# Kernel tuning notes

Measured on AMD Instinct MI355X. Metric: run time of the kernel, lower is better.

## Reference

```python
import jax, jax.numpy as jnp
import numpy as np
import math

B, S, D, H = 2, 2048, 1024, 16
DH = D // H


def setup_inputs() -> dict:
    key = jax.random.key(0)
    ks = jax.random.split(key, 10)
    scale = 1.0 / math.sqrt(D)
    inp = {
        "x": jax.random.normal(ks[0], (B, S, D), dtype=jnp.float32),
        "valid_nums": jax.random.randint(ks[1], (B,), 1, S + 1, dtype=jnp.int32),
        "Wq": jax.random.normal(ks[2], (D, D), dtype=jnp.float32) * scale,
        "bq": jnp.zeros((D,), dtype=jnp.float32),
        "Wk": jax.random.normal(ks[3], (D, D), dtype=jnp.float32) * scale,
        "bk": jnp.zeros((D,), dtype=jnp.float32),
        "Wv": jax.random.normal(ks[4], (D, D), dtype=jnp.float32) * scale,
        "bv": jnp.zeros((D,), dtype=jnp.float32),
        "Wo": jax.random.normal(ks[5], (D, D), dtype=jnp.float32) * scale,
        "bo": jnp.zeros((D,), dtype=jnp.float32),
    }
    return inp


def _split_heads(t):
    # (B, S, D) -> (B, H, S, DH)
    return t.reshape(B, S, H, DH).transpose(0, 2, 1, 3)


def reference(x, valid_nums, Wq, bq, Wk, bk, Wv, bv, Wo, bo):
    q = _split_heads(x @ Wq + bq)
    k = _split_heads(x @ Wk + bk)
    v = _split_heads(x @ Wv + bv)
    scores = jnp.einsum("bhqd,bhkd->bhqk", q, k) / math.sqrt(DH)  # (B,H,S,S)
    # length mask over keys: key j valid iff j < valid_nums[b]
    key_mask = jnp.arange(S)[None, :] < valid_nums[:, None]        # (B,S)
    scores = jnp.where(key_mask[:, None, None, :], scores, -jnp.inf)
    attn = jax.nn.softmax(scores, axis=-1)
    out = jnp.einsum("bhqk,bhkd->bhqd", attn, v)                   # (B,H,S,DH)
    out = out.transpose(0, 2, 1, 3).reshape(B, S, D)
    return out @ Wo + bo
```

## Files before the change

### kernel.cpp

```cpp
#include <hip/hip_runtime.h>
#include <hip/hip_bf16.h>
#include <math.h>

static constexpr int Bb = 2, Ss = 2048, Dd = 1024, Hh = 16, DHh = 64;
static constexpr int Mm = Bb * Ss;
static constexpr int Kk = Dd;

typedef __attribute__((ext_vector_type(8))) short bf16x8;
typedef __attribute__((ext_vector_type(4))) float f32x4;
typedef unsigned short us;

__device__ inline short f2b(float f) {
    __hip_bfloat16 h = __float2bfloat16(f);
    return *reinterpret_cast<short*>(&h);
}
__device__ inline float b2f(us u) {
    __hip_bfloat16 h = *reinterpret_cast<__hip_bfloat16*>(&u);
    return __bfloat162float(h);
}
__device__ inline unsigned pk2(float lo, float hi) {
    return ((unsigned)(us)f2b(hi) << 16) | (unsigned)(us)f2b(lo);
}
__device__ inline float ex2(float x) {
    return __builtin_amdgcn_exp2f(x);
}

__device__ inline void gload16(us* lds, const us* g) {
    __builtin_amdgcn_global_load_lds(
        (const __attribute__((address_space(1))) void*)g,
        (__attribute__((address_space(3))) void*)lds,
        16, 0, 0);
}

__global__ __launch_bounds__(256)
void xconv_kernel(const float* __restrict__ x, us* __restrict__ xb)
{
    const size_t i = ((size_t)blockIdx.x * 256 + threadIdx.x) * 8;
    float4 a = *(const float4*)(x + i);
    float4 b = *(const float4*)(x + i + 4);
    bf16x8 t;
    t[0] = f2b(a.x); t[1] = f2b(a.y); t[2] = f2b(a.z); t[3] = f2b(a.w);
    t[4] = f2b(b.x); t[5] = f2b(b.y); t[6] = f2b(b.z); t[7] = f2b(b.w);
    *(bf16x8*)(xb + i) = t;
}

__global__ __launch_bounds__(256)
void wtrans_kernel(const float* __restrict__ Wq, const float* __restrict__ Wk,
                   const float* __restrict__ Wv, const float* __restrict__ Wo,
                   us* __restrict__ Wt, us* __restrict__ Woth, us* __restrict__ Wotl)
{
    __shared__ float T[64][65];
    const int z = blockIdx.z;
    const float* W = (z == 0) ? Wq : (z == 1) ? Wk : (z == 2) ? Wv : Wo;
    const int split = (z == 3);
    us* dh = split ? Woth : (Wt + (size_t)z * Dd * Kk);
    us* dl = Wotl;

    const int n0 = blockIdx.x * 64, k0 = blockIdx.y * 64;
    const int tid = threadIdx.x;
    const int r = tid >> 2, c0 = (tid & 3) * 16;
#pragma unroll
    for (int j = 0; j < 4; ++j) {
        float4 v = *(const float4*)(W + (size_t)(k0 + r) * Dd + n0 + c0 + 4 * j);
        T[r][c0 + 4 * j + 0] = v.x;
        T[r][c0 + 4 * j + 1] = v.y;
        T[r][c0 + 4 * j + 2] = v.z;
        T[r][c0 + 4 * j + 3] = v.w;
    }
    __syncthreads();
    us hi[16], lo[16];
#pragma unroll
    for (int j = 0; j < 16; ++j) {
        float v = T[c0 + j][r];
        us h = (us)f2b(v);
        hi[j] = h;
        if (split) lo[j] = (us)f2b(v - b2f(h));
    }
    *(bf16x8*)&dh[(size_t)(n0 + r) * Kk + k0 + c0]     = *(bf16x8*)&hi[0];
    *(bf16x8*)&dh[(size_t)(n0 + r) * Kk + k0 + c0 + 8] = *(bf16x8*)&hi[8];
    if (split) {
        *(bf16x8*)&dl[(size_t)(n0 + r) * Kk + k0 + c0]     = *(bf16x8*)&lo[0];
        *(bf16x8*)&dl[(size_t)(n0 + r) * Kk + k0 + c0 + 8] = *(bf16x8*)&lo[8];
    }
}

__global__ __launch_bounds__(256)
void gemm_qkv_kernel(const us* __restrict__ xb, const us* __restrict__ Wt,
                     const float* __restrict__ bq, const float* __restrict__ bk,
                     const float* __restrict__ bv, us* __restrict__ QKV)
{
    __shared__ us As[2][128 * 64];
    __shared__ us Bs[2][128 * 64];
    const int tid = threadIdx.x;
    const int wave = tid >> 6, lane = tid & 63;
    const int wr = wave >> 1, wc = wave & 1;
    const int lg = lane >> 4, ll = lane & 15;
    const int col0 = blockIdx.x * 128;
    const int row0 = blockIdx.y * 128;

    f32x4 acc[4][4];
#pragma unroll
    for (int mt = 0; mt < 4; ++mt)
#pragma unroll
        for (int nt = 0; nt < 4; ++nt)
#pragma unroll
            for (int r = 0; r < 4; ++r) acc[mt][nt][r] = 0.f;

    const us* Ag = xb + (size_t)(row0 + wave * 32 + (lane >> 3)) * Kk + (lane & 7) * 8;
    const us* Bg = Wt + (size_t)(col0 + wave * 32 + (lane >> 3)) * Kk + (lane & 7) * 8;
    const int ldsb = (wave * 4) * 512;

#pragma unroll
    for (int i = 0; i < 4; ++i) {
        gload16(&As[0][ldsb + i * 512], Ag + (size_t)(i * 8) * Kk);
        gload16(&Bs[0][ldsb + i * 512], Bg + (size_t)(i * 8) * Kk);
    }
    __syncthreads();

    for (int it = 0; it < 16; ++it) {
        const int sb = it & 1;
        if (it < 15) {
            const int kn = (it + 1) * 64;
#pragma unroll
            for (int i = 0; i < 4; ++i) {
                gload16(&As[sb ^ 1][ldsb + i * 512], Ag + (size_t)(i * 8) * Kk + kn);
                gload16(&Bs[sb ^ 1][ldsb + i * 512], Bg + (size_t)(i * 8) * Kk + kn);
            }
        }
#pragma unroll
        for (int ks = 0; ks < 2; ++ks) {
            bf16x8 af[4], bfr[4];
#pragma unroll
            for (int mt = 0; mt < 4; ++mt)
                af[mt] = *(const bf16x8*)&As[sb][(wr * 64 + mt * 16 + ll) * 64 + ks * 32 + lg * 8];
#pragma unroll
            for (int nt = 0; nt < 4; ++nt)
                bfr[nt] = *(const bf16x8*)&Bs[sb][(wc * 64 + nt * 16 + ll) * 64 + ks * 32 + lg * 8];
#pragma unroll
            for (int mt = 0; mt < 4; ++mt)
#pragma unroll
                for (int nt = 0; nt < 4; ++nt)
                    acc[mt][nt] = __builtin_amdgcn_mfma_f32_16x16x32_bf16(af[mt], bfr[nt], acc[mt][nt], 0, 0, 0);
        }
        __syncthreads();
    }

    const int z = col0 >> 10;
    const int c0 = col0 & 1023;
    const float* bias = (z == 0) ? bq : (z == 1) ? bk : bv;
    const float osc = (z == 0) ? 0.125f * 1.44269504f : 1.0f;
    us* outz = QKV + (size_t)z * Mm * Dd;

    if (z == 2) {
#pragma unroll
        for (int mt = 0; mt < 4; ++mt)
#pragma unroll
            for (int nt = 0; nt < 4; ++nt) {
                int row = row0 + wr * 64 + mt * 16 + lg * 4;
                int col = c0 + wc * 64 + nt * 16 + ll;
                int b_ = row >> 11, s_ = row & 2047;
                float bv_ = bias[col];
                union { us u[4]; uint2 d2; } pk;
#pragma unroll
                for (int r = 0; r < 4; ++r) pk.u[r] = (us)f2b(acc[mt][nt][r] + bv_);
                *(uint2*)&outz[((size_t)(b_ * Hh * DHh) + col) * Ss + s_] = pk.d2;
            }
    } else {
#pragma unroll
        for (int mt = 0; mt < 4; ++mt)
#pragma unroll
            for (int nt = 0; nt < 4; ++nt)
#pragma unroll
                for (int r = 0; r < 4; ++r) {
                    int row = row0 + wr * 64 + mt * 16 + lg * 4 + r;
                    int col = c0 + wc * 64 + nt * 16 + ll;
                    float v = (acc[mt][nt][r] + bias[col]) * osc;
                    int b_ = row >> 11, s_ = row & 2047, h_ = col >> 6, d_ = col & 63;
                    outz[(((size_t)(b_ * Hh + h_)) * Ss + s_) * DHh + d_] = (us)f2b(v);
                }
    }
}

__global__ __launch_bounds__(256)
void gemm_final_kernel(const us* __restrict__ Oh, const us* __restrict__ Ol,
                       const us* __restrict__ Wth, const us* __restrict__ Wtl,
                       const float* __restrict__ bo, float* __restrict__ out)
{
    __shared__ us AhS[128 * 64];
    __shared__ us AlS[128 * 64];
    __shared__ us BhS[64 * 64];
    __shared__ us BlS[64 * 64];
    const int tid = threadIdx.x;
    const int wave = tid >> 6, lane = tid & 63;
    const int wr = wave >> 1, wc = wave & 1;
    const int lg = lane >> 4, ll = lane & 15;
    const int col0 = blockIdx.x * 64;
    const int row0 = blockIdx.y * 128;

    f32x4 acc[4][2];
#pragma unroll
    for (int mt = 0; mt < 4; ++mt)
#pragma unroll
        for (int nt = 0; nt < 2; ++nt)
#pragma unroll
            for (int r = 0; r < 4; ++r) acc[mt][nt][r] = 0.f;

    const size_t aoff = (size_t)(row0 + wave * 32 + (lane >> 3)) * Kk + (lane & 7) * 8;
    const size_t boff = (size_t)(col0 + wave * 16 + (lane >> 3)) * Kk + (lane & 7) * 8;
    const us* Ahg = Oh + aoff;
    const us* Alg = Ol + aoff;
    const us* Bhg = Wth + boff;
    const us* Blg = Wtl + boff;
    us* AhD = &AhS[(wave * 4) * 512];
    us* AlD = &AlS[(wave * 4) * 512];
    us* BhD = &BhS[(wave * 2) * 512];
    us* BlD = &BlS[(wave * 2) * 512];

    for (int k0 = 0; k0 < Kk; k0 += 64) {
        __syncthreads();
#pragma unroll
        for (int i = 0; i < 4; ++i) {
            gload16(AhD + i * 512, Ahg + (size_t)(i * 8) * Kk + k0);
            gload16(AlD + i * 512, Alg + (size_t)(i * 8) * Kk + k0);
        }
#pragma unroll
        for (int j = 0; j < 2; ++j) {
            gload16(BhD + j * 512, Bhg + (size_t)(j * 8) * Kk + k0);
            gload16(BlD + j * 512, Blg + (size_t)(j * 8) * Kk + k0);
        }
        __syncthreads();
#pragma unroll
        for (int ks = 0; ks < 2; ++ks) {
            bf16x8 ah[4], al[4], bh[2], bl[2];
#pragma unroll
            for (int mt = 0; mt < 4; ++mt) {
                ah[mt] = *(const bf16x8*)&AhS[(wr * 64 + mt * 16 + ll) * 64 + ks * 32 + lg * 8];
                al[mt] = *(const bf16x8*)&AlS[(wr * 64 + mt * 16 + ll) * 64 + ks * 32 + lg * 8];
            }
#pragma unroll
            for (int nt = 0; nt < 2; ++nt) {
                bh[nt] = *(const bf16x8*)&BhS[(wc * 32 + nt * 16 + ll) * 64 + ks * 32 + lg * 8];
                bl[nt] = *(const bf16x8*)&BlS[(wc * 32 + nt * 16 + ll) * 64 + ks * 32 + lg * 8];
            }
#pragma unroll
            for (int mt = 0; mt < 4; ++mt)
#pragma unroll
                for (int nt = 0; nt < 2; ++nt) {
                    acc[mt][nt] = __builtin_amdgcn_mfma_f32_16x16x32_bf16(ah[mt], bh[nt], acc[mt][nt], 0, 0, 0);
                    acc[mt][nt] = __builtin_amdgcn_mfma_f32_16x16x32_bf16(al[mt], bh[nt], acc[mt][nt], 0, 0, 0);
                    acc[mt][nt] = __builtin_amdgcn_mfma_f32_16x16x32_bf16(ah[mt], bl[nt], acc[mt][nt], 0, 0, 0);
                }
        }
    }

#pragma unroll
    for (int mt = 0; mt < 4; ++mt)
#pragma unroll
        for (int nt = 0; nt < 2; ++nt)
#pragma unroll
            for (int r = 0; r < 4; ++r) {
                int row = row0 + wr * 64 + mt * 16 + lg * 4 + r;
                int col = col0 + wc * 32 + nt * 16 + ll;
                out[(size_t)row * Dd + col] = acc[mt][nt][r] + bo[col];
            }
}

__global__ __launch_bounds__(512)
void attn_mfma_kernel(const us* __restrict__ Q, const us* __restrict__ K,
                      const us* __restrict__ Vt_g, const int* __restrict__ valid_nums,
                      us* __restrict__ Oh, us* __restrict__ Ol)
{
    const int id  = blockIdx.x;
    const int xcd = id & 7, grp = id >> 3;
    const int bh  = (grp >> 4) * 8 + xcd;
    const int qb  = grp & 15;
    const int b   = bh >> 4, h = bh & 15;
    const int q0  = qb * 128;

    const int tid  = threadIdx.x;
    const int wave = tid >> 6;
    const int lane = tid & 63;
    const int lg = lane >> 4;
    const int ll = lane & 15;

    const int nv = valid_nums[b];
    const int ntiles = (nv + 127) >> 7;

    const us* Qb = Q    + (size_t)bh * Ss * DHh;
    const us* Kb = K    + (size_t)bh * Ss * DHh;
    const us* Vb = Vt_g + (size_t)bh * DHh * Ss;

    __shared__ us Ks[128][72];
    __shared__ us Vs[64][136];

    bf16x8 qa[2];
    {
        const us* qrow = Qb + (size_t)(q0 + wave * 16 + ll) * DHh;
        qa[0] = *(const bf16x8*)(qrow + lg * 8);
        qa[1] = *(const bf16x8*)(qrow + 32 + lg * 8);
    }

    union { unsigned w[4]; bf16x8 v; } ones_u;
#pragma unroll
    for (int i = 0; i < 4; ++i) ones_u.w[i] = 0x3F803F80u;
    const bf16x8 vones = ones_u.v;

    f32x4 o[4], o4;
#pragma unroll
    for (int nt = 0; nt < 4; ++nt) { o[nt][0]=0.f; o[nt][1]=0.f; o[nt][2]=0.f; o[nt][3]=0.f; }
    o4[0]=0.f; o4[1]=0.f; o4[2]=0.f; o4[3]=0.f;
    float mq = -INFINITY;

    const int krow = tid >> 3;
    const int scol = (tid & 7) * 8;

    bf16x8 kr0 = *(const bf16x8*)(Kb + (size_t)krow * DHh + scol);
    bf16x8 kr1 = *(const bf16x8*)(Kb + (size_t)(64 + krow) * DHh + scol);
    bf16x8 vr0 = *(const bf16x8*)(Vb + (size_t)krow * Ss + scol);
    bf16x8 vr1 = *(const bf16x8*)(Vb + (size_t)krow * Ss + 64 + scol);

    const int l0 = (2 * (lg & 1)) * 16 + ll;
    const int l1 = l0 + 16;
    const bool hi = (lg & 2);

    for (int kt = 0; kt < ntiles; ++kt) {
        const int k0 = kt << 7;
        __syncthreads();
        *(bf16x8*)&Ks[krow][scol]      = kr0;
        *(bf16x8*)&Ks[krow + 64][scol] = kr1;
        *(bf16x8*)&Vs[krow][scol]      = vr0;
        *(bf16x8*)&Vs[krow][64 + scol] = vr1;
        __syncthreads();
        if (kt + 1 < ntiles) {
            const int kn = k0 + 128;
            kr0 = *(const bf16x8*)(Kb + (size_t)(kn + krow) * DHh + scol);
            kr1 = *(const bf16x8*)(Kb + (size_t)(kn + 64 + krow) * DHh + scol);
            vr0 = *(const bf16x8*)(Vb + (size_t)krow * Ss + kn + scol);
            vr1 = *(const bf16x8*)(Vb + (size_t)krow * Ss + kn + 64 + scol);
        }

        f32x4 s[8];
#pragma unroll
        for (int nt = 0; nt < 8; ++nt) { s[nt][0]=0.f; s[nt][1]=0.f; s[nt][2]=0.f; s[nt][3]=0.f; }
        __builtin_amdgcn_s_setprio(1);
#pragma unroll
        for (int ks = 0; ks < 2; ++ks) {
#pragma unroll
            for (int nt = 0; nt < 8; ++nt) {
                bf16x8 kf = *(const bf16x8*)&Ks[nt * 16 + ll][ks * 32 + lg * 8];
                s[nt] = __builtin_amdgcn_mfma_f32_16x16x32_bf16(kf, qa[ks], s[nt], 0, 0, 0);
            }
        }
        __builtin_amdgcn_s_setprio(0);

        float mx;
        if (k0 + 128 <= nv) {
            mx = -INFINITY;
#pragma unroll
            for (int nt = 0; nt < 8; ++nt)
#pragma unroll
                for (int r = 0; r < 4; ++r) mx = fmaxf(mx, s[nt][r]);
        } else {
            mx = -INFINITY;
#pragma unroll
            for (int nt = 0; nt < 8; ++nt)
#pragma unroll
                for (int r = 0; r < 4; ++r) {
                    int key = k0 + nt * 16 + lg * 4 + r;
                    float v = (key < nv) ? s[nt][r] : -INFINITY;
                    s[nt][r] = v;
                    mx = fmaxf(mx, v);
                }
        }
        mx = fmaxf(mx, __shfl_xor(mx, 16));
        mx = fmaxf(mx, __shfl_xor(mx, 32));

        const bool rescale = !__all(mx <= mq + 11.5f);
        if (rescale) {
            float mn = fmaxf(mq, mx);
            float corr = ex2(mq - mn);
            mq = mn;
            float corr4[4];
#pragma unroll
            for (int r = 0; r < 4; ++r) corr4[r] = __shfl(corr, lg * 16 + lg * 4 + r);
#pragma unroll
            for (int nt = 0; nt < 4; ++nt)
#pragma unroll
                for (int r = 0; r < 4; ++r) o[nt][r] *= corr4[r];
#pragma unroll
            for (int r = 0; r < 4; ++r) o4[r] *= corr4[r];
        }

#pragma unroll
        for (int g = 0; g < 4; ++g) {
            float pA[4], pB[4];
#pragma unroll
            for (int r = 0; r < 4; ++r) {
                pA[r] = ex2(s[2 * g][r] - mq);
                pB[r] = ex2(s[2 * g + 1][r] - mq);
            }
            unsigned dA0 = pk2(pA[0], pA[1]), dA1 = pk2(pA[2], pA[3]);
            unsigned dB0 = pk2(pB[0], pB[1]), dB1 = pk2(pB[2], pB[3]);

            unsigned a0 = (unsigned)__shfl((int)dA0, l0);
            unsigned a1 = (unsigned)__shfl((int)dA1, l0);
            unsigned a2 = (unsigned)__shfl((int)dA0, l1);
            unsigned a3 = (unsigned)__shfl((int)dA1, l1);
            unsigned b0 = (unsigned)__shfl((int)dB0, l0);
            unsigned b1 = (unsigned)__shfl((int)dB1, l0);
            unsigned b2 = (unsigned)__shfl((int)dB0, l1);
            unsigned b3 = (unsigned)__shfl((int)dB1, l1);
            union { unsigned w[4]; bf16x8 v; } pa;
            pa.w[0] = hi ? b0 : a0;
            pa.w[1] = hi ? b1 : a1;
            pa.w[2] = hi ? b2 : a2;
            pa.w[3] = hi ? b3 : a3;

            __builtin_amdgcn_s_setprio(1);
#pragma unroll
            for (int nt = 0; nt < 4; ++nt) {
                bf16x8 vb = *(const bf16x8*)&Vs[nt * 16 + ll][g * 32 + lg * 8];
                o[nt] = __builtin_amdgcn_mfma_f32_16x16x32_bf16(pa.v, vb, o[nt], 0, 0, 0);
            }
            o4 = __builtin_amdgcn_mfma_f32_16x16x32_bf16(pa.v, vones, o4, 0, 0, 0);
            __builtin_amdgcn_s_setprio(0);
        }
    }

#pragma unroll
    for (int r = 0; r < 4; ++r) {
        int row = q0 + wave * 16 + lg * 4 + r;
        float linv = 1.f / o4[r];
#pragma unroll
        for (int nt = 0; nt < 4; ++nt) {
            float val = o[nt][r] * linv;
            us uh = (us)f2b(val);
            float rem = val - b2f(uh);
            size_t base = ((size_t)b * Ss + row) * Dd + h * DHh + nt * 16 + ll;
            Oh[base] = uh;
            Ol[base] = (us)f2b(rem);
        }
    }
}

extern "C" void kernel_launch(void* const* d_in, const int* in_sizes, int n_in,
                              void* d_out, int out_size, void* d_ws, size_t ws_size,
                              hipStream_t stream) {
    const float* x     = (const float*)d_in[0];
    const int*   valid = (const int*)d_in[1];
    const float* Wq = (const float*)d_in[2];
    const float* bq = (const float*)d_in[3];
    const float* Wk = (const float*)d_in[4];
    const float* bk = (const float*)d_in[5];
    const float* Wv = (const float*)d_in[6];
    const float* bv = (const float*)d_in[7];
    const float* Wo = (const float*)d_in[8];
    const float* bo = (const float*)d_in[9];

    const size_t per = (size_t)Mm * Dd;
    const size_t wsz = (size_t)Dd * Kk;
    us* wsp  = (us*)d_ws;
    us* QKV  = wsp;
    us* Wt   = QKV + 3 * per;
    us* OhB  = Wt + 3 * wsz;
    us* OlB  = OhB + per;
    us* Woth = OlB + per;
    us* Wotl = Woth + wsz;
    us* xb   = Wotl + wsz;

    xconv_kernel<<<(Mm * Kk) / (256 * 8), 256, 0, stream>>>(x, xb);

    wtrans_kernel<<<dim3(Dd / 64, Kk / 64, 4), 256, 0, stream>>>(
        Wq, Wk, Wv, Wo, Wt, Woth, Wotl);

    gemm_qkv_kernel<<<dim3(3 * Dd / 128, Mm / 128), 256, 0, stream>>>(
        xb, Wt, bq, bk, bv, QKV);

    attn_mfma_kernel<<<(Ss / 128) * (Bb * Hh), 512, 0, stream>>>(
        QKV, QKV + per, QKV + 2 * per, valid, OhB, OlB);

    gemm_final_kernel<<<dim3(Dd / 64, Mm / 128), 256, 0, stream>>>(
        OhB, OlB, Woth, Wotl, bo, (float*)d_out);
}
```

Baseline: 155.6 us.

## Merge prep kernels, remap GEMM blocks per XCD, single-buffer QKV GEMM LDS

Combines the x conversion and weight transpose kernels into one launch, which removes a kernel launch and the gap between them. Remaps the block indices of both GEMMs so that blocks on the same XCD (selected by blockIdx & 7) share column tiles, aiming for better L2 reuse of the weights. It also replaces the QKV GEMM's double-buffered LDS prefetch with a single buffer and two barriers per iteration. That halves LDS use and may raise occupancy, but loads no longer overlap with MFMA work.

```diff
diff --git a/kernel.cpp b/kernel.cpp
--- a/kernel.cpp
+++ b/kernel.cpp
@@ -33,31 +33,35 @@
 }
 
 __global__ __launch_bounds__(256)
-void xconv_kernel(const float* __restrict__ x, us* __restrict__ xb)
-{
-    const size_t i = ((size_t)blockIdx.x * 256 + threadIdx.x) * 8;
-    float4 a = *(const float4*)(x + i);
-    float4 b = *(const float4*)(x + i + 4);
-    bf16x8 t;
-    t[0] = f2b(a.x); t[1] = f2b(a.y); t[2] = f2b(a.z); t[3] = f2b(a.w);
-    t[4] = f2b(b.x); t[5] = f2b(b.y); t[6] = f2b(b.z); t[7] = f2b(b.w);
-    *(bf16x8*)(xb + i) = t;
-}
-
-__global__ __launch_bounds__(256)
-void wtrans_kernel(const float* __restrict__ Wq, const float* __restrict__ Wk,
-                   const float* __restrict__ Wv, const float* __restrict__ Wo,
-                   us* __restrict__ Wt, us* __restrict__ Woth, us* __restrict__ Wotl)
+void prep_kernel(const float* __restrict__ x, us* __restrict__ xb,
+                 const float* __restrict__ Wq, const float* __restrict__ Wk,
+                 const float* __restrict__ Wv, const float* __restrict__ Wo,
+                 us* __restrict__ Wt, us* __restrict__ Woth, us* __restrict__ Wotl)
 {
     __shared__ float T[64][65];
-    const int z = blockIdx.z;
+    const int id = blockIdx.x;
+    const int tid = threadIdx.x;
+
+    if (id < 2048) {
+        const size_t i = ((size_t)id * 256 + tid) * 8;
+        float4 a = *(const float4*)(x + i);
+        float4 b = *(const float4*)(x + i + 4);
+        bf16x8 t;
+        t[0] = f2b(a.x); t[1] = f2b(a.y); t[2] = f2b(a.z); t[3] = f2b(a.w);
+        t[4] = f2b(b.x); t[5] = f2b(b.y); t[6] = f2b(b.z); t[7] = f2b(b.w);
+        *(bf16x8*)(xb + i) = t;
+        return;
+    }
+
+    const int w = id - 2048;
+    const int z = w >> 8;
+    const int rem = w & 255;
+    const int n0 = (rem & 15) * 64, k0 = (rem >> 4) * 64;
     const float* W = (z == 0) ? Wq : (z == 1) ? Wk : (z == 2) ? Wv : Wo;
     const int split = (z == 3);
     us* dh = split ? Woth : (Wt + (size_t)z * Dd * Kk);
     us* dl = Wotl;
 
-    const int n0 = blockIdx.x * 64, k0 = blockIdx.y * 64;
-    const int tid = threadIdx.x;
     const int r = tid >> 2, c0 = (tid & 3) * 16;
 #pragma unroll
     for (int j = 0; j < 4; ++j) {
@@ -89,14 +93,18 @@
                      const float* __restrict__ bq, const float* __restrict__ bk,
                      const float* __restrict__ bv, us* __restrict__ QKV)
 {
-    __shared__ us As[2][128 * 64];
-    __shared__ us Bs[2][128 * 64];
+    __shared__ us As[128 * 64];
+    __shared__ us Bs[128 * 64];
     const int tid = threadIdx.x;
     const int wave = tid >> 6, lane = tid & 63;
     const int wr = wave >> 1, wc = wave & 1;
     const int lg = lane >> 4, ll = lane & 15;
-    const int col0 = blockIdx.x * 128;
-    const int row0 = blockIdx.y * 128;
+
+    const int id = blockIdx.x;
+    const int xcd = id & 7;
+    const int j = id >> 3;
+    const int col0 = (xcd * 3 + j % 3) * 128;
+    const int row0 = (j / 3) * 128;
 
     f32x4 acc[4][4];
 #pragma unroll
@@ -108,41 +116,32 @@
 
     const us* Ag = xb + (size_t)(row0 + wave * 32 + (lane >> 3)) * Kk + (lane & 7) * 8;
     const us* Bg = Wt + (size_t)(col0 + wave * 32 + (lane >> 3)) * Kk + (lane & 7) * 8;
-    const int ldsb = (wave * 4) * 512;
-
-#pragma unroll
-    for (int i = 0; i < 4; ++i) {
-        gload16(&As[0][ldsb + i * 512], Ag + (size_t)(i * 8) * Kk);
-        gload16(&Bs[0][ldsb + i * 512], Bg + (size_t)(i * 8) * Kk);
-    }
-    __syncthreads();
-
-    for (int it = 0; it < 16; ++it) {
-        const int sb = it & 1;
-        if (it < 15) {
-            const int kn = (it + 1) * 64;
-#pragma unroll
-            for (int i = 0; i < 4; ++i) {
-                gload16(&As[sb ^ 1][ldsb + i * 512], Ag + (size_t)(i * 8) * Kk + kn);
-                gload16(&Bs[sb ^ 1][ldsb + i * 512], Bg + (size_t)(i * 8) * Kk + kn);
-            }
-        }
+    us* Ad = &As[(wave * 4) * 512];
+    us* Bd = &Bs[(wave * 4) * 512];
+
+    for (int k0 = 0; k0 < Kk; k0 += 64) {
+        __syncthreads();
+#pragma unroll
+        for (int i = 0; i < 4; ++i) {
+            gload16(Ad + i * 512, Ag + (size_t)(i * 8) * Kk + k0);
+            gload16(Bd + i * 512, Bg + (size_t)(i * 8) * Kk + k0);
+        }
+        __syncthreads();
 #pragma unroll
         for (int ks = 0; ks < 2; ++ks) {
             bf16x8 af[4], bfr[4];
 #pragma unroll
             for (int mt = 0; mt < 4; ++mt)
-                af[mt] = *(const bf16x8*)&As[sb][(wr * 64 + mt * 16 + ll) * 64 + ks * 32 + lg * 8];
+                af[mt] = *(const bf16x8*)&As[(wr * 64 + mt * 16 + ll) * 64 + ks * 32 + lg * 8];
 #pragma unroll
             for (int nt = 0; nt < 4; ++nt)
-                bfr[nt] = *(const bf16x8*)&Bs[sb][(wc * 64 + nt * 16 + ll) * 64 + ks * 32 + lg * 8];
+                bfr[nt] = *(const bf16x8*)&Bs[(wc * 64 + nt * 16 + ll) * 64 + ks * 32 + lg * 8];
 #pragma unroll
             for (int mt = 0; mt < 4; ++mt)
 #pragma unroll
                 for (int nt = 0; nt < 4; ++nt)
                     acc[mt][nt] = __builtin_amdgcn_mfma_f32_16x16x32_bf16(af[mt], bfr[nt], acc[mt][nt], 0, 0, 0);
         }
-        __syncthreads();
     }
 
     const int z = col0 >> 10;
@@ -194,8 +193,12 @@
     const int wave = tid >> 6, lane = tid & 63;
     const int wr = wave >> 1, wc = wave & 1;
     const int lg = lane >> 4, ll = lane & 15;
-    const int col0 = blockIdx.x * 64;
-    const int row0 = blockIdx.y * 128;
+
+    const int id = blockIdx.x;
+    const int xcd = id & 7;
+    const int j = id >> 3;
+    const int col0 = (xcd * 2 + (j & 1)) * 64;
+    const int row0 = (j >> 1) * 128;
 
     f32x4 acc[4][2];
 #pragma unroll
@@ -224,9 +227,9 @@
             gload16(AlD + i * 512, Alg + (size_t)(i * 8) * Kk + k0);
         }
 #pragma unroll
-        for (int j = 0; j < 2; ++j) {
-            gload16(BhD + j * 512, Bhg + (size_t)(j * 8) * Kk + k0);
-            gload16(BlD + j * 512, Blg + (size_t)(j * 8) * Kk + k0);
+        for (int j2 = 0; j2 < 2; ++j2) {
+            gload16(BhD + j2 * 512, Bhg + (size_t)(j2 * 8) * Kk + k0);
+            gload16(BlD + j2 * 512, Blg + (size_t)(j2 * 8) * Kk + k0);
         }
         __syncthreads();
 #pragma unroll
@@ -468,17 +471,14 @@
     us* Wotl = Woth + wsz;
     us* xb   = Wotl + wsz;
 
-    xconv_kernel<<<(Mm * Kk) / (256 * 8), 256, 0, stream>>>(x, xb);
-
-    wtrans_kernel<<<dim3(Dd / 64, Kk / 64, 4), 256, 0, stream>>>(
-        Wq, Wk, Wv, Wo, Wt, Woth, Wotl);
-
-    gemm_qkv_kernel<<<dim3(3 * Dd / 128, Mm / 128), 256, 0, stream>>>(
-        xb, Wt, bq, bk, bv, QKV);
+    prep_kernel<<<2048 + 1024, 256, 0, stream>>>(
+        x, xb, Wq, Wk, Wv, Wo, Wt, Woth, Wotl);
+
+    gemm_qkv_kernel<<<768, 256, 0, stream>>>(xb, Wt, bq, bk, bv, QKV);
 
     attn_mfma_kernel<<<(Ss / 128) * (Bb * Hh), 512, 0, stream>>>(
         QKV, QKV + per, QKV + 2 * per, valid, OhB, OlB);
 
-    gemm_final_kernel<<<dim3(Dd / 64, Mm / 128), 256, 0, stream>>>(
+    gemm_final_kernel<<<512, 256, 0, stream>>>(
         OhB, OlB, Woth, Wotl, bo, (float*)d_out);
 }
```

New measurement: 142.0 us. 1.1x faster.
